# Performance work log

Hardware: AMD Instinct MI355X
Metric: run time of the kernel (lower is better)

## Reference

```python
import jax, jax.numpy as jnp
import numpy as np

FP8_MAX = 448.0  # torch.finfo(float8_e4m3fn).max


def quant_fp8(x):
    # dynamic per-tensor quantization: amax -> scale -> cast to fp8
    amax = jnp.max(jnp.abs(x)).astype(jnp.float32)
    scale = jnp.minimum(FP8_MAX / jnp.maximum(amax, 1e-12), FP8_MAX)
    x_fp8 = jnp.clip(x * scale, -FP8_MAX, FP8_MAX).astype(jnp.float8_e4m3fn)
    return x_fp8, 1.0 / scale  # (fp8 data, dequant scale)


def setup_inputs() -> dict:
    key = jax.random.key(0)
    k1, k2, k3 = jax.random.split(key, 3)
    B, S, IN, OUT = 4, 8192, 1024, 1024
    input = jax.random.normal(k1, (B, S, IN), dtype=jnp.float32)
    # kaiming_uniform_(a=sqrt(5)) -> uniform(-1/sqrt(in), 1/sqrt(in))
    bound = 1.0 / np.sqrt(IN)
    weight = jax.random.uniform(k2, (OUT, IN), dtype=jnp.float32, minval=-bound, maxval=bound)
    bias = jax.random.uniform(k3, (OUT,), dtype=jnp.float32, minval=-bound, maxval=bound)
    return {"input": input, "weight": weight, "bias": bias}


def reference(input, weight, bias):
    prev_shape = input.shape
    x2d = input.reshape(-1, weight.shape[1])  # [T, in]
    w_fp8, w_scale = quant_fp8(weight)
    x_fp8, x_scale = quant_fp8(x2d)
    # bias add, bf16 output
    acc = jnp.matmul(x_fp8.astype(jnp.float32), w_fp8.astype(jnp.float32).T)
    out2d = (acc * (x_scale * w_scale) + bias).astype(jnp.bfloat16)
    out = out2d.reshape(*prev_shape[:-1], weight.shape[0]).astype(input.dtype)
    return out
```

## Files before the change

kernel.cpp:

```cpp
#include <hip/hip_runtime.h>
#include <hip/hip_bf16.h>

typedef float f32x4 __attribute__((ext_vector_type(4)));
typedef long lx2 __attribute__((ext_vector_type(2)));

#define FP8_MAX_F 448.0f

__device__ __forceinline__ float wave_max(float m) {
#pragma unroll
    for (int off = 32; off > 0; off >>= 1)
        m = fmaxf(m, __shfl_xor(m, off));
    return m;
}

__global__ void amax2_kernel(const float* __restrict__ x, long nx,
                             const float* __restrict__ w, long nw,
                             float* __restrict__ px, float* __restrict__ pw,
                             int ga) {
    __shared__ float red[4];
    const float* src; long n; float* dst; int bid, blocks;
    if ((int)blockIdx.x < ga) { src = x; n = nx; dst = px; bid = blockIdx.x; blocks = ga; }
    else { src = w; n = nw; dst = pw; bid = blockIdx.x - ga; blocks = gridDim.x - ga; }

    const long stride = (long)blocks * blockDim.x * 16;
    long i = ((long)bid * blockDim.x + threadIdx.x) * 16;
    float m = 0.0f;
    for (; i < n; i += stride) {
        f32x4 v0 = *(const f32x4*)(src + i);
        f32x4 v1 = *(const f32x4*)(src + i + 4);
        f32x4 v2 = *(const f32x4*)(src + i + 8);
        f32x4 v3 = *(const f32x4*)(src + i + 12);
        float m0 = fmaxf(fmaxf(fabsf(v0.x), fabsf(v0.y)), fmaxf(fabsf(v0.z), fabsf(v0.w)));
        float m1 = fmaxf(fmaxf(fabsf(v1.x), fabsf(v1.y)), fmaxf(fabsf(v1.z), fabsf(v1.w)));
        float m2 = fmaxf(fmaxf(fabsf(v2.x), fabsf(v2.y)), fmaxf(fabsf(v2.z), fabsf(v2.w)));
        float m3 = fmaxf(fmaxf(fabsf(v3.x), fabsf(v3.y)), fmaxf(fabsf(v3.z), fabsf(v3.w)));
        m = fmaxf(m, fmaxf(fmaxf(m0, m1), fmaxf(m2, m3)));
    }
    m = wave_max(m);
    const int wave = threadIdx.x >> 6;
    if ((threadIdx.x & 63) == 0) red[wave] = m;
    __syncthreads();
    if (threadIdx.x == 0)
        dst[bid] = fmaxf(fmaxf(red[0], red[1]), fmaxf(red[2], red[3]));
}

__global__ void amax_final_kernel(const float* __restrict__ px, int npx,
                                  const float* __restrict__ pw, int npw,
                                  unsigned* __restrict__ amax) {
    __shared__ float red[4];
    const float* p; int n;
    if (blockIdx.x == 0) { p = px; n = npx; } else { p = pw; n = npw; }
    float m = 0.0f;
    for (int i = threadIdx.x; i < n; i += blockDim.x) m = fmaxf(m, p[i]);
    m = wave_max(m);
    const int wave = threadIdx.x >> 6;
    if ((threadIdx.x & 63) == 0) red[wave] = m;
    __syncthreads();
    if (threadIdx.x == 0) {
        m = fmaxf(fmaxf(red[0], red[1]), fmaxf(red[2], red[3]));
        amax[blockIdx.x] = __float_as_uint(m);
    }
}

__global__ void quant2_kernel(const float* __restrict__ x, long nx8,
                              const float* __restrict__ w, long nw8,
                              const unsigned* __restrict__ amax_bits,
                              unsigned* __restrict__ qx, unsigned* __restrict__ qw,
                              int ga) {
    const float* src; long n8; unsigned* q; int bid, blocks; float a;
    if ((int)blockIdx.x < ga) { src = x; n8 = nx8; q = qx; bid = blockIdx.x; blocks = ga;
                                a = __uint_as_float(amax_bits[0]); }
    else { src = w; n8 = nw8; q = qw; bid = blockIdx.x - ga; blocks = gridDim.x - ga;
           a = __uint_as_float(amax_bits[1]); }
    const float scale = fminf(FP8_MAX_F / fmaxf(a, 1e-12f), FP8_MAX_F);

    const long stride = (long)blocks * blockDim.x;
    for (long i = (long)bid * blockDim.x + threadIdx.x; i < n8; i += stride) {
        f32x4 v0 = *(const f32x4*)(src + i * 8);
        f32x4 v1 = *(const f32x4*)(src + i * 8 + 4);
        float c0 = fminf(fmaxf(v0.x * scale, -FP8_MAX_F), FP8_MAX_F);
        float c1 = fminf(fmaxf(v0.y * scale, -FP8_MAX_F), FP8_MAX_F);
        float c2 = fminf(fmaxf(v0.z * scale, -FP8_MAX_F), FP8_MAX_F);
        float c3 = fminf(fmaxf(v0.w * scale, -FP8_MAX_F), FP8_MAX_F);
        float c4 = fminf(fmaxf(v1.x * scale, -FP8_MAX_F), FP8_MAX_F);
        float c5 = fminf(fmaxf(v1.y * scale, -FP8_MAX_F), FP8_MAX_F);
        float c6 = fminf(fmaxf(v1.z * scale, -FP8_MAX_F), FP8_MAX_F);
        float c7 = fminf(fmaxf(v1.w * scale, -FP8_MAX_F), FP8_MAX_F);
        int r0 = __builtin_amdgcn_cvt_pk_fp8_f32(c0, c1, 0, false);
        r0 = __builtin_amdgcn_cvt_pk_fp8_f32(c2, c3, r0, true);
        int r1 = __builtin_amdgcn_cvt_pk_fp8_f32(c4, c5, 0, false);
        r1 = __builtin_amdgcn_cvt_pk_fp8_f32(c6, c7, r1, true);
        uint2 rr; rr.x = (unsigned)r0; rr.y = (unsigned)r1;
        *(uint2*)(q + i * 2) = rr;
    }
}

__global__ __launch_bounds__(512, 2) void gemm_fp8_kernel(
    const unsigned char* __restrict__ Xq,
    const unsigned char* __restrict__ Wq,
    const float* __restrict__ bias,
    const unsigned* __restrict__ amax_bits,
    float* __restrict__ out,
    int M, int N, int K, int nbn)
{
    __shared__ unsigned char ldsA[3][16384];
    __shared__ unsigned char ldsB[3][16384];

    const int tid  = threadIdx.x;
    const int lane = tid & 63;
    const int wave = tid >> 6;
    const int wm128 = (wave >> 2) * 128;
    const int wn64  = (wave & 3) * 64;

    const int l15 = lane & 15;
    const int lhi = lane >> 4;

    const int cpx = gridDim.x >> 3;
    const int wg  = ((int)blockIdx.x & 7) * cpx + ((int)blockIdx.x >> 3);
    const int bn = wg % nbn;
    const int bm = wg / nbn;
    const int rowStart = bm << 8;
    const int colStart = bn << 8;

    const int aoff0 = lhi * 4096 + (wm128 + l15) * 16;
    const int boff  = lhi * 4096 + (wn64 + l15) * 16;

    const size_t aoffs = (size_t)(rowStart + (tid & 255)) * K + (tid >> 8) * 16;
    const size_t boffs = (size_t)(colStart + (tid & 255)) * K + (tid >> 8) * 16;
    const int tid16 = tid * 16;

    f32x4 acc[8][4] = {};

#define STAGE_A(t, sl)                                                                          \
    do {                                                                                        \
        const size_t kk_ = (size_t)(t) * 64;                                                    \
        __builtin_amdgcn_global_load_lds(                                                       \
            (const __attribute__((address_space(1))) void*)(Xq + aoffs + kk_),                  \
            (__attribute__((address_space(3))) void*)(&ldsA[sl][tid16]), 16, 0, 0);             \
        __builtin_amdgcn_global_load_lds(                                                       \
            (const __attribute__((address_space(1))) void*)(Xq + aoffs + 32 + kk_),             \
            (__attribute__((address_space(3))) void*)(&ldsA[sl][8192 + tid16]), 16, 0, 0);      \
    } while (0)

#define STAGE_B(t, sl)                                                                          \
    do {                                                                                        \
        const size_t kk_ = (size_t)(t) * 64;                                                    \
        __builtin_amdgcn_global_load_lds(                                                       \
            (const __attribute__((address_space(1))) void*)(Wq + boffs + kk_),                  \
            (__attribute__((address_space(3))) void*)(&ldsB[sl][tid16]), 16, 0, 0);             \
        __builtin_amdgcn_global_load_lds(                                                       \
            (const __attribute__((address_space(1))) void*)(Wq + boffs + 32 + kk_),             \
            (__attribute__((address_space(3))) void*)(&ldsB[sl][8192 + tid16]), 16, 0, 0);      \
    } while (0)

#define MFMA32(AF, BF, MO)                                                                      \
    do {                                                                                        \
        __builtin_amdgcn_s_setprio(1);                                                          \
        _Pragma("unroll")                                                                       \
        for (int ks_ = 0; ks_ < 2; ++ks_)                                                       \
            _Pragma("unroll")                                                                   \
            for (int mi_ = 0; mi_ < 4; ++mi_)                                                   \
                _Pragma("unroll")                                                               \
                for (int ni_ = 0; ni_ < 4; ++ni_)                                               \
                    acc[(MO) + mi_][ni_] = __builtin_amdgcn_mfma_f32_16x16x32_fp8_fp8(          \
                        AF[mi_][ks_], BF[ni_][ks_], acc[(MO) + mi_][ni_], 0, 0, 0);             \
        __builtin_amdgcn_s_setprio(0);                                                          \
    } while (0)

#define BODY(t, sA, AF, BF, AF2, BF2)                                                           \
    do {                                                                                        \
        const int s_  = (sA);                                                                   \
        const int s1_ = (s_ + 1 >= 3) ? s_ - 2 : s_ + 1;                                        \
        const int s2_ = (s_ + 2 >= 3) ? s_ - 1 : s_ + 2;                                        \
        const unsigned char* bA_ = &ldsA[s_][0];                                                \
        _Pragma("unroll")                                                                       \
        for (int q_ = 0; q_ < 4; ++q_)                                                          \
            ag[q_] = *(const lx2*)(bA_ + aoff0 + 1024 + q_ * 256);                              \
        if ((t) + 2 < nT) { STAGE_A((t) + 2, s2_); STAGE_B((t) + 2, s2_); }                     \
        asm volatile("s_waitcnt lgkmcnt(4)" ::: "memory");       \
        __builtin_amdgcn_sched_barrier(0);                                                      \
        MFMA32(AF, BF, 0);                                                                      \
        asm volatile("s_waitcnt lgkmcnt(0)" ::: "memory");       \
        if ((t) + 2 < nT) asm volatile("s_waitcnt vmcnt(4)" ::: "memory");                      \
        else              asm volatile("s_waitcnt vmcnt(0)" ::: "memory");                      \
        __builtin_amdgcn_s_barrier();                                                           \
        __builtin_amdgcn_sched_barrier(0);                                                      \
        if ((t) + 1 < nT) {                                                                     \
            const unsigned char* nA_ = &ldsA[s1_][0];                                           \
            const unsigned char* nB_ = &ldsB[s1_][0];                                           \
            _Pragma("unroll")                                                                   \
            for (int q_ = 0; q_ < 4; ++q_) {                                                    \
                AF2[q_] = *(const lx2*)(nA_ + aoff0 + q_ * 256);                                \
                BF2[q_] = *(const lx2*)(nB_ + boff + q_ * 256);                                 \
            }                                                                                   \
        }                                                                                       \
        MFMA32(ag, BF, 4);                                                                      \
    } while (0)

    STAGE_A(0, 0); STAGE_B(0, 0);
    STAGE_A(1, 1); STAGE_B(1, 1);
    asm volatile("s_waitcnt vmcnt(4)" ::: "memory");
    __builtin_amdgcn_s_barrier();
    __builtin_amdgcn_sched_barrier(0);

    lx2 afA[4], bfA[4], afB[4], bfB[4], ag[4];
#pragma unroll
    for (int q_ = 0; q_ < 4; ++q_) {
        afA[q_] = *(const lx2*)(&ldsA[0][aoff0 + q_ * 256]);
        bfA[q_] = *(const lx2*)(&ldsB[0][boff + q_ * 256]);
    }

    const int nT = K >> 6;
    int s = 0;
#pragma unroll 1
    for (int t = 0; t < nT; t += 2) {
        const int sn = (s + 1 >= 3) ? s - 2 : s + 1;
        BODY(t,     s,  afA, bfA, afB, bfB);
        BODY(t + 1, sn, afB, bfB, afA, bfA);
        s = (s + 2 >= 3) ? s - 1 : s + 2;
    }
#undef BODY
#undef MFMA32
#undef STAGE_A
#undef STAGE_B

    const float ax = __uint_as_float(amax_bits[0]);
    const float aw = __uint_as_float(amax_bits[1]);
    const float sx = fminf(FP8_MAX_F / fmaxf(ax, 1e-12f), FP8_MAX_F);
    const float sw = fminf(FP8_MAX_F / fmaxf(aw, 1e-12f), FP8_MAX_F);
    const float sc = (1.0f / sx) * (1.0f / sw);

    const int lhi4 = lhi * 4;
#pragma unroll
    for (int ni = 0; ni < 4; ++ni) {
        const int col = colStart + wn64 + ni * 16 + l15;
        const float bv = bias[col];
#pragma unroll
        for (int mi = 0; mi < 8; ++mi) {
            const size_t rbase = (size_t)(rowStart + wm128 + mi * 16 + lhi4) * N + col;
#pragma unroll
            for (int j = 0; j < 4; ++j) {
                float t = acc[mi][ni][j] * sc;
                t = t + bv;
                out[rbase + (size_t)j * N] = __bfloat162float(__float2bfloat16(t));
            }
        }
    }
}

extern "C" void kernel_launch(void* const* d_in, const int* in_sizes, int n_in,
                              void* d_out, int out_size, void* d_ws, size_t ws_size,
                              hipStream_t stream) {
    const float* input  = (const float*)d_in[0];
    const float* weight = (const float*)d_in[1];
    const float* bias   = (const float*)d_in[2];
    float* out = (float*)d_out;

    const int K = 1024;
    const int N = in_sizes[2];
    const long nX = in_sizes[0];
    const long nW = (long)N * K;
    const int M = (int)(nX / K);

    const int GA = 1984;
    const int GW = 64;

    unsigned char* ws = (unsigned char*)d_ws;
    unsigned* amax = (unsigned*)ws;
    unsigned char* Xq = ws + 256;
    unsigned char* Wq = Xq + (size_t)M * K;
    float* px = (float*)(Wq + (size_t)N * K);
    float* pw = px + GA;

    amax2_kernel<<<GA + GW, 256, 0, stream>>>(input, nX, weight, nW, px, pw, GA);
    amax_final_kernel<<<2, 256, 0, stream>>>(px, GA, pw, GW, amax);

    quant2_kernel<<<2048, 256, 0, stream>>>(input, nX / 8, weight, nW / 8, amax,
                                            (unsigned*)Xq, (unsigned*)Wq, GA);

    const int nbn = N / 256;
    const int nwg = (M / 256) * nbn;
    gemm_fp8_kernel<<<dim3(nwg), dim3(512), 0, stream>>>(Xq, Wq, bias, amax, out, M, N, K, nbn);
}
```

Measured before the change: 128.4 us.

## Switch GEMM to 32x32x64 scaled fp8 MFMA with per-stage fragment reads

Replaces the 16x16x32 fp8 MFMA tiles with the gfx950 scaled 32x32x64 f8f6f4 MFMA, using unit scales, so each instruction covers a full 64-deep K step. The LDS fragment layout, accumulator shape and epilogue row mapping are rewritten to match the 32x32 output layout. The split A-fragment prefetch is dropped in favor of reading all fragments for the next stage after the barrier. Launch bounds drop to one block per CU minimum, giving the compiler more registers at some cost to occupancy. The aim is to cut MFMA instruction count and LDS read overhead, but the simpler schedule overlaps LDS reads with MFMAs less.

```diff
diff --git a/kernel.cpp b/kernel.cpp
--- a/kernel.cpp
+++ b/kernel.cpp
@@ -2,9 +2,12 @@
 #include <hip/hip_bf16.h>
 
 typedef float f32x4 __attribute__((ext_vector_type(4)));
-typedef long lx2 __attribute__((ext_vector_type(2)));
+typedef float f32x16 __attribute__((ext_vector_type(16)));
+typedef int   i32x4  __attribute__((ext_vector_type(4)));
+typedef int   i32x8  __attribute__((ext_vector_type(8)));
 
 #define FP8_MAX_F 448.0f
+#define SCL1 0x7F7F7F7Fu
 
 __device__ __forceinline__ float wave_max(float m) {
 #pragma unroll
@@ -95,7 +98,7 @@
     }
 }
 
-__global__ __launch_bounds__(512, 2) void gemm_fp8_kernel(
+__global__ __launch_bounds__(512, 1) void gemm_fp8_kernel(
     const unsigned char* __restrict__ Xq,
     const unsigned char* __restrict__ Wq,
     const float* __restrict__ bias,
@@ -112,8 +115,8 @@
     const int wm128 = (wave >> 2) * 128;
     const int wn64  = (wave & 3) * 64;
 
-    const int l15 = lane & 15;
-    const int lhi = lane >> 4;
+    const int l31 = lane & 31;
+    const int g   = lane >> 5;
 
     const int cpx = gridDim.x >> 3;
     const int wg  = ((int)blockIdx.x & 7) * cpx + ((int)blockIdx.x >> 3);
@@ -122,14 +125,15 @@
     const int rowStart = bm << 8;
     const int colStart = bn << 8;
 
-    const int aoff0 = lhi * 4096 + (wm128 + l15) * 16;
-    const int boff  = lhi * 4096 + (wn64 + l15) * 16;
+    const int aoffL = (2 * g) * 4096 + (wm128 + l31) * 16;
+    const int boffL = (2 * g) * 4096 + (wn64  + l31) * 16;
 
     const size_t aoffs = (size_t)(rowStart + (tid & 255)) * K + (tid >> 8) * 16;
     const size_t boffs = (size_t)(colStart + (tid & 255)) * K + (tid >> 8) * 16;
     const int tid16 = tid * 16;
 
-    f32x4 acc[8][4] = {};
+    union Frag { i32x8 v; struct { i32x4 lo, hi; } h; };
+    f32x16 acc[4][2] = {};
 
 #define STAGE_A(t, sl)                                                                          \
     do {                                                                                        \
@@ -153,48 +157,45 @@
             (__attribute__((address_space(3))) void*)(&ldsB[sl][8192 + tid16]), 16, 0, 0);      \
     } while (0)
 
-#define MFMA32(AF, BF, MO)                                                                      \
+#define RD_FRAGS(sl, FA, FB)                                                                    \
+    do {                                                                                        \
+        const unsigned char* rA_ = &ldsA[sl][0];                                                \
+        const unsigned char* rB_ = &ldsB[sl][0];                                                \
+        _Pragma("unroll")                                                                       \
+        for (int mt_ = 0; mt_ < 4; ++mt_) {                                                     \
+            FA[mt_].h.lo = *(const i32x4*)(rA_ + aoffL + mt_ * 512);                            \
+            FA[mt_].h.hi = *(const i32x4*)(rA_ + aoffL + 4096 + mt_ * 512);                     \
+        }                                                                                       \
+        _Pragma("unroll")                                                                       \
+        for (int nt_ = 0; nt_ < 2; ++nt_) {                                                     \
+            FB[nt_].h.lo = *(const i32x4*)(rB_ + boffL + nt_ * 512);                            \
+            FB[nt_].h.hi = *(const i32x4*)(rB_ + boffL + 4096 + nt_ * 512);                     \
+        }                                                                                       \
+    } while (0)
+
+#define MFMA8(FA, FB)                                                                           \
     do {                                                                                        \
         __builtin_amdgcn_s_setprio(1);                                                          \
         _Pragma("unroll")                                                                       \
-        for (int ks_ = 0; ks_ < 2; ++ks_)                                                       \
+        for (int mt_ = 0; mt_ < 4; ++mt_)                                                       \
             _Pragma("unroll")                                                                   \
-            for (int mi_ = 0; mi_ < 4; ++mi_)                                                   \
-                _Pragma("unroll")                                                               \
-                for (int ni_ = 0; ni_ < 4; ++ni_)                                               \
-                    acc[(MO) + mi_][ni_] = __builtin_amdgcn_mfma_f32_16x16x32_fp8_fp8(          \
-                        AF[mi_][ks_], BF[ni_][ks_], acc[(MO) + mi_][ni_], 0, 0, 0);             \
+            for (int nt_ = 0; nt_ < 2; ++nt_)                                                   \
+                acc[mt_][nt_] = __builtin_amdgcn_mfma_scale_f32_32x32x64_f8f6f4(                \
+                    FA[mt_].v, FB[nt_].v, acc[mt_][nt_], 0, 0, 0, SCL1, 0, SCL1);               \
         __builtin_amdgcn_s_setprio(0);                                                          \
     } while (0)
 
-#define BODY(t, sA, AF, BF, AF2, BF2)                                                           \
-    do {                                                                                        \
-        const int s_  = (sA);                                                                   \
-        const int s1_ = (s_ + 1 >= 3) ? s_ - 2 : s_ + 1;                                        \
-        const int s2_ = (s_ + 2 >= 3) ? s_ - 1 : s_ + 2;                                        \
-        const unsigned char* bA_ = &ldsA[s_][0];                                                \
-        _Pragma("unroll")                                                                       \
-        for (int q_ = 0; q_ < 4; ++q_)                                                          \
-            ag[q_] = *(const lx2*)(bA_ + aoff0 + 1024 + q_ * 256);                              \
-        if ((t) + 2 < nT) { STAGE_A((t) + 2, s2_); STAGE_B((t) + 2, s2_); }                     \
-        asm volatile("s_waitcnt lgkmcnt(4)" ::: "memory");       \
+#define BODY(t, sNext, sStage, FA, FB, FA2, FB2)                                                \
+    do {                                                                                        \
+        if ((t) + 2 < nT) { STAGE_A((t) + 2, sStage); STAGE_B((t) + 2, sStage); }               \
+        asm volatile("s_waitcnt lgkmcnt(0)" ::: "memory");                                      \
         __builtin_amdgcn_sched_barrier(0);                                                      \
-        MFMA32(AF, BF, 0);                                                                      \
-        asm volatile("s_waitcnt lgkmcnt(0)" ::: "memory");       \
+        MFMA8(FA, FB);                                                                          \
         if ((t) + 2 < nT) asm volatile("s_waitcnt vmcnt(4)" ::: "memory");                      \
         else              asm volatile("s_waitcnt vmcnt(0)" ::: "memory");                      \
         __builtin_amdgcn_s_barrier();                                                           \
         __builtin_amdgcn_sched_barrier(0);                                                      \
-        if ((t) + 1 < nT) {                                                                     \
-            const unsigned char* nA_ = &ldsA[s1_][0];                                           \
-            const unsigned char* nB_ = &ldsB[s1_][0];                                           \
-            _Pragma("unroll")                                                                   \
-            for (int q_ = 0; q_ < 4; ++q_) {                                                    \
-                AF2[q_] = *(const lx2*)(nA_ + aoff0 + q_ * 256);                                \
-                BF2[q_] = *(const lx2*)(nB_ + boff + q_ * 256);                                 \
-            }                                                                                   \
-        }                                                                                       \
-        MFMA32(ag, BF, 4);                                                                      \
+        if ((t) + 1 < nT) RD_FRAGS(sNext, FA2, FB2);                                            \
     } while (0)
 
     STAGE_A(0, 0); STAGE_B(0, 0);
@@ -203,24 +204,22 @@
     __builtin_amdgcn_s_barrier();
     __builtin_amdgcn_sched_barrier(0);
 
-    lx2 afA[4], bfA[4], afB[4], bfB[4], ag[4];
-#pragma unroll
-    for (int q_ = 0; q_ < 4; ++q_) {
-        afA[q_] = *(const lx2*)(&ldsA[0][aoff0 + q_ * 256]);
-        bfA[q_] = *(const lx2*)(&ldsB[0][boff + q_ * 256]);
-    }
+    Frag faA[4], fbA[2], faB[4], fbB[2];
+    RD_FRAGS(0, faA, fbA);
 
     const int nT = K >> 6;
     int s = 0;
 #pragma unroll 1
     for (int t = 0; t < nT; t += 2) {
-        const int sn = (s + 1 >= 3) ? s - 2 : s + 1;
-        BODY(t,     s,  afA, bfA, afB, bfB);
-        BODY(t + 1, sn, afB, bfB, afA, bfA);
-        s = (s + 2 >= 3) ? s - 1 : s + 2;
+        const int s1 = (s + 1 >= 3) ? s - 2 : s + 1;
+        const int s2 = (s + 2 >= 3) ? s - 1 : s + 2;
+        BODY(t,     s1, s2, faA, fbA, faB, fbB);
+        BODY(t + 1, s2, s,  faB, fbB, faA, fbA);
+        s = s2;
     }
 #undef BODY
-#undef MFMA32
+#undef MFMA8
+#undef RD_FRAGS
 #undef STAGE_A
 #undef STAGE_B
 
@@ -230,19 +229,18 @@
     const float sw = fminf(FP8_MAX_F / fmaxf(aw, 1e-12f), FP8_MAX_F);
     const float sc = (1.0f / sx) * (1.0f / sw);
 
-    const int lhi4 = lhi * 4;
-#pragma unroll
-    for (int ni = 0; ni < 4; ++ni) {
-        const int col = colStart + wn64 + ni * 16 + l15;
+#pragma unroll
+    for (int nt = 0; nt < 2; ++nt) {
+        const int col = colStart + wn64 + nt * 32 + l31;
         const float bv = bias[col];
 #pragma unroll
-        for (int mi = 0; mi < 8; ++mi) {
-            const size_t rbase = (size_t)(rowStart + wm128 + mi * 16 + lhi4) * N + col;
-#pragma unroll
-            for (int j = 0; j < 4; ++j) {
-                float t = acc[mi][ni][j] * sc;
-                t = t + bv;
-                out[rbase + (size_t)j * N] = __bfloat162float(__float2bfloat16(t));
+        for (int mt = 0; mt < 4; ++mt) {
+#pragma unroll
+            for (int r = 0; r < 16; ++r) {
+                const int row = rowStart + wm128 + mt * 32 + (r & 3) + 8 * (r >> 2) + 4 * g;
+                float tt = acc[mt][nt][r] * sc;
+                tt = tt + bv;
+                out[(size_t)row * N + col] = __bfloat162float(__float2bfloat16(tt));
             }
         }
     }
```

Result: faster. 119.5 us (-6.9%).
